# Kernel tuning notes

Hardware: AMD Instinct MI355X
Metric: run time of the kernel (lower is better)

The kernel has to match this reference:

```python
import jax, jax.numpy as jnp
import numpy as np

B, T, C, E, K = 8, 2048, 1024, 8, 2
CAP = int(T / E * 1.25)  # expert capacity per batch row = 320


def setup_inputs() -> dict:
    key = jax.random.key(0)
    ks = jax.random.split(key, 6)
    s = lambda k, shape, fan: jax.random.normal(k, shape, jnp.float32) / np.sqrt(fan)
    return dict(
        x=jax.random.normal(ks[0], (B, T, C), jnp.float32),
        rw1=s(ks[1], (C, 4 * C), C), rb1=jnp.zeros((4 * C,), jnp.float32),
        rw2=s(ks[2], (4 * C, 4 * C), 4 * C), rb2=jnp.zeros((4 * C,), jnp.float32),
        rw3=s(ks[3], (4 * C, E), 4 * C), rb3=jnp.zeros((E,), jnp.float32),
        ew1=s(ks[4], (E, C, 4 * C), C), eb1=jnp.zeros((E, 4 * C), jnp.float32),
        ew2=s(ks[5], (E, 4 * C, C), 4 * C), eb2=jnp.zeros((E, C), jnp.float32),
    )


def reference(x, rw1, rb1, rw2, rb2, rw3, rb3, ew1, eb1, ew2, eb2):
    # Router (dropout is identity in eval): MLP -> softmax over experts
    h = jax.nn.relu(x @ rw1 + rb1)
    h = jax.nn.relu(h @ rw2 + rb2)
    probs = jax.nn.softmax(h @ rw3 + rb3, axis=-1)        # [B,T,E]
    topk_p, topk_e = jax.lax.top_k(probs, K)              # [B,T,K]

    b_ids = jnp.broadcast_to(jnp.arange(B)[:, None], (B, T))
    out = jnp.zeros_like(x)
    # Loop over small fixed number of experts (mirrors per-rank expert compute)
    for e in range(E):
        sel = (topk_e == e)                               # [B,T,K]
        mask = sel.any(-1)                                # token routed to expert e
        gate = (topk_p * sel).sum(-1)                     # unnormalized top-k prob
        pos = jnp.cumsum(mask, axis=1) - 1                # slot within capacity buffer
        keep = mask & (pos < CAP)                         # capacity truncation (drop overflow)
        pos_s = jnp.where(keep, pos, CAP)                 # CAP is out-of-range -> dropped
        # Dispatch: scatter kept tokens into [B, CAP, C] capacity-padded buffer
        buf = jnp.zeros((B, CAP, C), x.dtype).at[b_ids, pos_s].set(x, mode='drop')
        # Expert FFN on padded buffer
        y = jax.nn.relu(buf @ ew1[e] + eb1[e]) @ ew2[e] + eb2[e]
        # Combine: gather back to token positions, weight by gate
        g = y[b_ids, jnp.where(keep, pos, 0)]
        out = out + gate[..., None] * jnp.where(keep[..., None], g, jnp.zeros((), x.dtype))
    return out
```

## Files before the change

### kernel.cpp

```cpp
#include <hip/hip_runtime.h>
#include <stdint.h>

typedef _Float16 f16;
typedef _Float16 half8 __attribute__((ext_vector_type(8)));
typedef float f32x4 __attribute__((ext_vector_type(4)));

#define NF_MAX 2048
#define THETA  0.02f

__device__ __forceinline__ void gload16(const void* g, void* l) {
  __builtin_amdgcn_global_load_lds(
      (const __attribute__((address_space(1))) void*)g,
      (__attribute__((address_space(3))) void*)l, 16, 0, 0);
}

#define BAR() do { __builtin_amdgcn_s_barrier(); __builtin_amdgcn_sched_barrier(0); } while (0)
#define WAIT_VM8() do { asm volatile("s_waitcnt vmcnt(8)" ::: "memory"); __builtin_amdgcn_sched_barrier(0); } while (0)
#define WAIT_VM0() do { asm volatile("s_waitcnt vmcnt(0)" ::: "memory"); __builtin_amdgcn_sched_barrier(0); } while (0)

template<int EPI, bool SPLIT3>
__launch_bounds__(512, 2)
__global__ void gemm256(const f16* __restrict__ A0, const f16* __restrict__ A1,
                        const f16* __restrict__ B0, const f16* __restrict__ B1,
                        int N, int Kd, int lda, int ldb,
                        const int* __restrict__ rowsrcA, const f16* __restrict__ zeroPage,
                        const float* __restrict__ bias, int bias_stride, int rows_per_exp,
                        f16* __restrict__ oH, int ldo, float* __restrict__ oAcc,
                        const float* __restrict__ w3, float* __restrict__ oLog,
                        const int* __restrict__ nfp)
{
  __shared__ f16 lds[4 * 8192 * 2 + 512];
  f16* sA = lds;
  f16* sB = lds + 4 * 8192;
  f16* sDummy = lds + 8 * 8192;

  const int tid  = threadIdx.x;
  const int lane = tid & 63, w = tid >> 6;
  const int wm = w >> 2, wn = w & 3;

  const int gx  = gridDim.x;
  const int nwg = gx * gridDim.y;
  const int bid = blockIdx.y * gx + blockIdx.x;
  const int swz = (bid & 7) * (nwg >> 3) + (bid >> 3);
  const int by  = swz / gx, bx = swz - by * gx;
  const int m0  = by * 256, n0 = bx * 256;
  const int k0  = blockIdx.z * Kd;

  if (nfp) {
    int nf = *nfp; nf = nf < NF_MAX ? nf : NF_MAX;
    const int lim = (nf + 255) & ~255;
    if (m0 >= lim) return;
  }

  int e = 0;
  if (rows_per_exp > 0) e = m0 / rows_per_exp;
  const f16* Bh = B0 + (size_t)e * N * ldb;

  const int nk  = Kd >> 6;
  const int NIT = SPLIT3 ? 3 * nk : nk;

  const int sr  = lane & 15;
  const int sk8 = lane >> 4;

  size_t aoff[2], boff[2];
  bool az[2] = { false, false };
  #pragma unroll
  for (int jj = 0; jj < 2; ++jj) {
    const int arow = m0 + (jj * 8 + w) * 16 + sr;
    if (rowsrcA) {
      const int rs = rowsrcA[arow];
      az[jj] = (rs < 0);
      aoff[jj] = az[jj] ? 0 : (size_t)rs * lda;
    } else {
      aoff[jj] = (size_t)arow * lda;
    }
    boff[jj] = (size_t)(n0 + (jj * 8 + w) * 16 + sr) * ldb;
  }

  auto stageA = [&](const f16* base, int kk, int kc, f16* slotBase, bool valid) {
    #pragma unroll
    for (int jj = 0; jj < 2; ++jj) {
      const int mt = jj * 8 + w;
      f16* dst = valid ? (slotBase + mt * 512) : sDummy;
      const f16* src = az[jj] ? zeroPage
                              : base + aoff[jj] + (k0 + kk + kc * 32 + sk8 * 8);
      gload16(src, dst);
    }
  };
  auto stageB = [&](const f16* base, int kk, int kc, f16* slotBase, bool valid) {
    #pragma unroll
    for (int jj = 0; jj < 2; ++jj) {
      const int mt = jj * 8 + w;
      f16* dst = valid ? (slotBase + mt * 512) : sDummy;
      const f16* src = base + boff[jj] + (k0 + kk + kc * 32 + sk8 * 8);
      gload16(src, dst);
    }
  };

  struct It { const f16* Ab; const f16* Bb; int kk, kin, pass; };
  const f16* Ab0 = SPLIT3 ? A1 : A0;
  auto advance = [&](It& s) {
    if (s.kin + 1 < nk) { s.kin++; }
    else if (SPLIT3 && s.pass < 2) {
      s.kin = 0; s.pass++;
      s.Ab = (s.pass == 0) ? A1 : A0;
      s.Bb = (s.pass == 1) ? B1 : Bh;
    }
    s.kk = s.kin << 6;
  };
  It it1 = { Ab0, Bh, 64, 1, 0 };
  It it2 = { Ab0, Bh, 128, 2, 0 };

  stageA(Ab0, 0, 0, &sA[0], true);
  stageB(Bh,  0, 0, &sB[0], true);
  stageA(Ab0, 0, 1, &sA[8192], true);
  stageB(Bh,  0, 1, &sB[8192], true);
  stageA(it1.Ab, it1.kk, 0, &sA[2 * 8192], true);
  stageB(it1.Bb, it1.kk, 0, &sB[2 * 8192], true);
  WAIT_VM8();
  BAR();

  f32x4 acc[8][4] = {};
  const int aBase = wm * 8;
  const int bBase = wn * 4;

  auto mfma16 = [&](half8* af, half8* bf, int moff) {
    __builtin_amdgcn_s_setprio(1);
    #pragma unroll
    for (int mi = 0; mi < 4; ++mi)
      #pragma unroll
      for (int ni = 0; ni < 4; ++ni)
        acc[moff + mi][ni] = __builtin_amdgcn_mfma_f32_16x16x32_f16(
            af[mi], bf[ni], acc[moff + mi][ni], 0, 0, 0);
    __builtin_amdgcn_s_setprio(0);
  };
  auto rdA = [&](half8* dst, int slot, int mtb) {
    #pragma unroll
    for (int mi = 0; mi < 4; ++mi)
      dst[mi] = *(const half8*)&sA[slot * 8192 + (mtb + mi) * 512 + lane * 8];
  };
  auto rdB = [&](half8* dst, int slot) {
    #pragma unroll
    for (int ni = 0; ni < 4; ++ni)
      dst[ni] = *(const half8*)&sB[slot * 8192 + (bBase + ni) * 512 + lane * 8];
  };

  for (int t = 0; t < NIT; ++t) {
    const int sa0 = (2 * t) & 3, sa1 = sa0 ^ 1;
    const bool v1 = (t + 1 < NIT), v2 = (t + 2 < NIT);

    if (SPLIT3 && t == 2 * nk) {
      #pragma unroll
      for (int mi = 0; mi < 8; ++mi)
        #pragma unroll
        for (int ni = 0; ni < 4; ++ni)
          acc[mi][ni] = acc[mi][ni] * 2.44140625e-4f;
    }

    half8 aF[4], bF[4], aG[4];

    rdA(aF, sa0, aBase);
    rdB(bF, sa0);
    stageA(it1.Ab, it1.kk, 1, &sA[(sa0 ^ 3) * 8192], v1);
    BAR();
    mfma16(aF, bF, 0);
    BAR();

    rdA(aG, sa0, aBase + 4);
    stageB(it1.Bb, it1.kk, 1, &sB[(sa0 ^ 3) * 8192], v1);
    WAIT_VM8();
    BAR();
    mfma16(aG, bF, 4);
    BAR();

    rdA(aF, sa1, aBase);
    rdB(bF, sa1);
    stageA(it2.Ab, it2.kk, 0, &sA[sa0 * 8192], v2);
    BAR();
    mfma16(aF, bF, 0);
    BAR();

    rdA(aG, sa1, aBase + 4);
    stageB(it2.Bb, it2.kk, 0, &sB[sa0 * 8192], v2);
    WAIT_VM8();
    BAR();
    mfma16(aG, bF, 4);
    BAR();

    it1 = it2;
    advance(it2);
  }
  WAIT_VM0();

  float bv[4] = { 0.f, 0.f, 0.f, 0.f };
  if (bias) {
    #pragma unroll
    for (int ni = 0; ni < 4; ++ni) {
      const int col = n0 + wn * 64 + ni * 16 + (lane & 15);
      bv[ni] = bias[(size_t)e * bias_stride + col];
    }
  }

  if (EPI == 2) {
    f32x4 wlo[4], whi[4];
    #pragma unroll
    for (int ni = 0; ni < 4; ++ni) {
      const int col = n0 + wn * 64 + ni * 16 + (lane & 15);
      wlo[ni] = *(const f32x4*)(w3 + (size_t)col * 8);
      whi[ni] = *(const f32x4*)(w3 + (size_t)col * 8 + 4);
    }
    const int p = (n0 >> 8) * 4 + wn;
    #pragma unroll
    for (int mi = 0; mi < 8; ++mi) {
      #pragma unroll
      for (int r = 0; r < 4; ++r) {
        const int row = m0 + wm * 128 + mi * 16 + (lane >> 4) * 4 + r;
        f32x4 plo = {}, phi = {};
        #pragma unroll
        for (int ni = 0; ni < 4; ++ni) {
          const float v = fmaxf(acc[mi][ni][r] + bv[ni], 0.f);
          plo += v * wlo[ni];
          phi += v * whi[ni];
        }
        #pragma unroll
        for (int msk = 1; msk < 16; msk <<= 1) {
          #pragma unroll
          for (int q = 0; q < 4; ++q) {
            plo[q] += __shfl_xor(plo[q], msk);
            phi[q] += __shfl_xor(phi[q], msk);
          }
        }
        if ((lane & 15) == 0) {
          float* dst = oLog + ((size_t)p * 4096 + row) * 8;
          *(f32x4*)dst = plo;
          *(f32x4*)(dst + 4) = phi;
        }
      }
    }
  } else {
    #pragma unroll
    for (int mi = 0; mi < 8; ++mi) {
      #pragma unroll
      for (int r = 0; r < 4; ++r) {
        const int row = m0 + wm * 128 + mi * 16 + (lane >> 4) * 4 + r;
        #pragma unroll
        for (int ni = 0; ni < 4; ++ni) {
          const int col = n0 + wn * 64 + ni * 16 + (lane & 15);
          if (EPI == 3) {
            atomicAdd(&oAcc[(size_t)row * ldo + col], acc[mi][ni][r]);
          } else {
            float v = acc[mi][ni][r] + bv[ni];
            if (EPI == 0) v = fmaxf(v, 0.f);
            oH[(size_t)row * ldo + col] = (f16)v;
          }
        }
      }
    }
  }
}

__global__ void split_x(const float* __restrict__ x, f16* __restrict__ hi,
                        f16* __restrict__ lo, int n)
{
  const int i = blockIdx.x * 256 + threadIdx.x;
  if (i * 8 >= n) return;
  const f32x4 a = ((const f32x4*)x)[2 * i];
  const f32x4 b = ((const f32x4*)x)[2 * i + 1];
  half8 h, l;
  #pragma unroll
  for (int j = 0; j < 4; ++j) {
    float v = a[j]; f16 hh = (f16)v;
    h[j] = hh; l[j] = (f16)((v - (float)hh) * 4096.0f);
    v = b[j]; hh = (f16)v;
    h[4 + j] = hh; l[4 + j] = (f16)((v - (float)hh) * 4096.0f);
  }
  ((half8*)hi)[i] = h;
  ((half8*)lo)[i] = l;
}

template<bool SPLIT>
__global__ void transpose_conv(const float* __restrict__ in, f16* __restrict__ oh,
                               f16* __restrict__ ol, int R, int Cc)
{
  __shared__ float tile[64][65];
  const size_t boff = (size_t)blockIdx.z * R * Cc;
  in += boff; oh += boff;
  if (SPLIT) ol += boff;
  const int c0 = blockIdx.x * 64, r0 = blockIdx.y * 64;
  #pragma unroll
  for (int i = 0; i < 16; ++i) {
    const int idx = i * 256 + threadIdx.x;
    const int r = idx >> 6, c = idx & 63;
    tile[r][c] = in[(size_t)(r0 + r) * Cc + (c0 + c)];
  }
  __syncthreads();
  #pragma unroll
  for (int i = 0; i < 16; ++i) {
    const int idx = i * 256 + threadIdx.x;
    const int ro = idx >> 6, co = idx & 63;
    const float v = tile[co][ro];
    const f16 h = (f16)v;
    const size_t o = (size_t)(c0 + ro) * R + (r0 + co);
    oh[o] = h;
    if (SPLIT) ol[o] = (f16)((v - (float)h) * 4096.0f);
  }
}

__global__ void topk_flag(const float* __restrict__ part, const float* __restrict__ b3,
                          int tok0, int* __restrict__ eidx, float* __restrict__ gval,
                          int* __restrict__ flags, int* __restrict__ nfc)
{
  const int tl = blockIdx.x * 256 + threadIdx.x;
  const int t  = tok0 + tl;
  float l[8];
  #pragma unroll
  for (int e = 0; e < 8; ++e) l[e] = b3[e];
  for (int p = 0; p < 64; ++p) {
    const float* src = part + ((size_t)p * 4096 + tl) * 8;
    const f32x4 a = *(const f32x4*)src;
    const f32x4 b = *(const f32x4*)(src + 4);
    #pragma unroll
    for (int q = 0; q < 4; ++q) { l[q] += a[q]; l[4 + q] += b[q]; }
  }
  float mx = l[0];
  #pragma unroll
  for (int e = 1; e < 8; ++e) mx = fmaxf(mx, l[e]);
  float ex[8], s = 0.f;
  #pragma unroll
  for (int e = 0; e < 8; ++e) { ex[e] = expf(l[e] - mx); s += ex[e]; }
  float p1 = -1.f, p2 = -1.f; int e1 = 0, e2 = 0;
  #pragma unroll
  for (int e = 0; e < 8; ++e) {
    const float pe = ex[e] / s;
    if (pe > p1)      { p2 = p1; e2 = e1; p1 = pe; e1 = e; }
    else if (pe > p2) { p2 = pe; e2 = e; }
  }
  eidx[t * 2] = e1; eidx[t * 2 + 1] = e2;
  gval[t * 2] = p1; gval[t * 2 + 1] = p2;
  float l1 = -1e30f, l2 = -1e30f, l3 = -1e30f;
  #pragma unroll
  for (int e = 0; e < 8; ++e) {
    const float le = l[e];
    if (le > l1)      { l3 = l2; l2 = l1; l1 = le; }
    else if (le > l2) { l3 = l2; l2 = le; }
    else if (le > l3) { l3 = le; }
  }
  if (l2 - l3 < THETA) {
    const int s0 = atomicAdd(nfc, 1);
    if (s0 < NF_MAX) flags[s0] = t;
  }
}

__global__ void post1(const float* __restrict__ h1r, const float* __restrict__ b1,
                      f16* __restrict__ hh, f16* __restrict__ hl,
                      const int* __restrict__ nfc)
{
  int nf = *nfc; nf = nf < NF_MAX ? nf : NF_MAX;
  const int lim = (nf + 255) & ~255;
  const int row = blockIdx.x;
  if (row >= lim) return;
  const int j = blockIdx.y * 2048 + threadIdx.x * 8;
  const float* src = h1r + (size_t)row * 4096 + j;
  const f32x4 a = *(const f32x4*)src;
  const f32x4 b = *(const f32x4*)(src + 4);
  half8 h, l;
  #pragma unroll
  for (int k = 0; k < 4; ++k) {
    float v = fmaxf(a[k] + b1[j + k], 0.f);
    f16 x = (f16)v; h[k] = x; l[k] = (f16)((v - (float)x) * 4096.0f);
    v = fmaxf(b[k] + b1[j + 4 + k], 0.f);
    x = (f16)v; h[4 + k] = x; l[4 + k] = (f16)((v - (float)x) * 4096.0f);
  }
  *(half8*)(hh + (size_t)row * 4096 + j) = h;
  *(half8*)(hl + (size_t)row * 4096 + j) = l;
}

__global__ void logits_exact(const float* __restrict__ h2r, const float* __restrict__ b2,
                             const float* __restrict__ w3, const float* __restrict__ b3,
                             const int* __restrict__ flags, const int* __restrict__ nfc,
                             int* __restrict__ eidx, float* __restrict__ gval)
{
  const int srow = blockIdx.x;
  int nf = *nfc; nf = nf < NF_MAX ? nf : NF_MAX;
  if (srow >= nf) return;
  const float* hrow = h2r + (size_t)srow * 4096;
  double p[8];
  #pragma unroll
  for (int e = 0; e < 8; ++e) p[e] = 0.0;
  for (int i = 0; i < 16; ++i) {
    const int k = i * 256 + threadIdx.x;
    const double h = (double)fmaxf(hrow[k] + b2[k], 0.f);
    const float* wp = w3 + (size_t)k * 8;
    #pragma unroll
    for (int e = 0; e < 8; ++e) p[e] += h * (double)wp[e];
  }
  #pragma unroll
  for (int e = 0; e < 8; ++e)
    for (int off = 32; off > 0; off >>= 1)
      p[e] += __shfl_down(p[e], off);
  __shared__ double sp[4][8];
  const int lane = threadIdx.x & 63, wv = threadIdx.x >> 6;
  if (lane == 0) {
    #pragma unroll
    for (int e = 0; e < 8; ++e) sp[wv][e] = p[e];
  }
  __syncthreads();
  if (threadIdx.x == 0) {
    float l[8];
    #pragma unroll
    for (int e = 0; e < 8; ++e)
      l[e] = (float)(sp[0][e] + sp[1][e] + sp[2][e] + sp[3][e] + (double)b3[e]);
    float mx = l[0];
    for (int e = 1; e < 8; ++e) mx = fmaxf(mx, l[e]);
    float ex[8], s = 0.f;
    for (int e = 0; e < 8; ++e) { ex[e] = expf(l[e] - mx); s += ex[e]; }
    float p1 = -1.f, p2 = -1.f; int e1 = 0, e2 = 0;
    for (int e = 0; e < 8; ++e) {
      const float pe = ex[e] / s;
      if (pe > p1)      { p2 = p1; e2 = e1; p1 = pe; e1 = e; }
      else if (pe > p2) { p2 = pe; e2 = e; }
    }
    const int tok = flags[srow];
    eidx[tok * 2] = e1; eidx[tok * 2 + 1] = e2;
    gval[tok * 2] = p1; gval[tok * 2 + 1] = p2;
  }
}

__global__ void route_scan(const int* __restrict__ eidx, const float* __restrict__ gval,
                           int* __restrict__ idxl, float* __restrict__ gatel,
                           int* __restrict__ cnt, int* __restrict__ rowsrc,
                           int* __restrict__ tokslot)
{
  const int pair = blockIdx.x;
  const int e = pair >> 3, b = pair & 7;
  const int lane = threadIdx.x;
  int running = 0;
  for (int t0 = 0; t0 < 2048; t0 += 64) {
    const int t = t0 + lane;
    const int i2 = (b * 2048 + t) * 2;
    const int m0 = (eidx[i2] == e), m1 = (eidx[i2 + 1] == e);
    const int m = m0 | m1;
    const float g = m0 ? gval[i2] : (m1 ? gval[i2 + 1] : 0.f);
    const unsigned long long bal = __ballot(m);
    const int pos = running + __popcll(bal & ((1ull << lane) - 1ull));
    if (m && pos < 320) {
      idxl[pair * 320 + pos] = t;
      gatel[pair * 320 + pos] = g;
      const int slot = pair * 320 + pos;
      rowsrc[slot] = b * 2048 + t;
      tokslot[(b * 2048 + t) * 2 + (m0 ? 0 : 1)] = slot;
    }
    running += __popcll(bal);
  }
  if (lane == 0) cnt[pair] = running < 320 ? running : 320;
}

__global__ void combine(const f16* __restrict__ yb, const int* __restrict__ tokslot,
                        const float* __restrict__ gval, float* __restrict__ out)
{
  const int t = blockIdx.x;
  const int s0 = tokslot[t * 2], s1 = tokslot[t * 2 + 1];
  const float g0 = gval[t * 2], g1 = gval[t * 2 + 1];
  float a[8] = {};
  if (s0 >= 0) {
    const half8 y = ((const half8*)(yb + (size_t)s0 * 1024))[threadIdx.x];
    #pragma unroll
    for (int k = 0; k < 8; ++k) a[k] += g0 * (float)y[k];
  }
  if (s1 >= 0) {
    const half8 y = ((const half8*)(yb + (size_t)s1 * 1024))[threadIdx.x];
    #pragma unroll
    for (int k = 0; k < 8; ++k) a[k] += g1 * (float)y[k];
  }
  float* dst = out + (size_t)t * 1024 + threadIdx.x * 8;
  f32x4 lo = { a[0], a[1], a[2], a[3] }, hi = { a[4], a[5], a[6], a[7] };
  *(f32x4*)dst = lo;
  *(f32x4*)(dst + 4) = hi;
}

extern "C" void kernel_launch(void* const* d_in, const int* in_sizes, int n_in,
                              void* d_out, int out_size, void* d_ws, size_t ws_size,
                              hipStream_t stream)
{
  (void)in_sizes; (void)n_in; (void)out_size;
  const float* x   = (const float*)d_in[0];
  const float* rw1 = (const float*)d_in[1];
  const float* rb1 = (const float*)d_in[2];
  const float* rw2 = (const float*)d_in[3];
  const float* rb2 = (const float*)d_in[4];
  const float* rw3 = (const float*)d_in[5];
  const float* rb3 = (const float*)d_in[6];
  const float* ew1 = (const float*)d_in[7];
  const float* eb1 = (const float*)d_in[8];
  const float* ew2 = (const float*)d_in[9];
  const float* eb2 = (const float*)d_in[10];

  constexpr size_t MB = 1024ull * 1024ull;
  constexpr size_t KB = 1024ull;
  char* ws = (char*)d_ws;
  if (ws_size < 401 * MB) return;

  f16*   ew1t  = (f16*)(ws);
  f16*   ew2t  = (f16*)(ws + 64 * MB);
  f16*   xhi   = (f16*)(ws + 128 * MB);
  char*  S     = ws + 160 * MB;
  int*   eidx   = (int*)(S);
  float* gval   = (float*)(S + 128 * KB);
  int*   idxl   = (int*)(S + 256 * KB);
  float* gatel  = (float*)(S + 352 * KB);
  int*   cnt    = (int*)(S + 448 * KB);
  int*   nfc    = (int*)(S + 452 * KB);
  int*   flags  = (int*)(S + 456 * KB);
  int*   tokslot= (int*)(S + 464 * KB);
  int*   rowsrc = (int*)(S + 592 * KB);
  f16*   zeros  = (f16*)(S + 688 * KB);
  f16*   xlo    = (f16*)(ws + 162 * MB);
  f16*   rw1thi = (f16*)(ws + 194 * MB);
  f16*   rw1tlo = (f16*)(ws + 202 * MB);
  f16*   rw2thi = (f16*)(ws + 210 * MB);
  f16*   rw2tlo = (f16*)(ws + 242 * MB);
  f16*   h1f    = (f16*)(ws + 274 * MB);
  float* h1r    = (float*)(ws + 274 * MB);
  float* h2r    = (float*)(ws + 306 * MB);
  f16*   h1rh   = (f16*)(ws + 338 * MB);
  f16*   h1rl   = (f16*)(ws + 354 * MB);
  float* part   = (float*)(ws + 390 * MB);
  f16*   h_e    = (f16*)(ws + 162 * MB);
  f16*   yb     = (f16*)(ws + 322 * MB);

  hipMemsetAsync(nfc, 0, 4, stream);
  hipMemsetAsync(flags, 0, 8 * KB, stream);
  hipMemsetAsync(tokslot, 0xFF, 128 * KB, stream);
  hipMemsetAsync(rowsrc, 0xFF, 80 * KB, stream);
  hipMemsetAsync(zeros, 0, 16 * KB, stream);

  split_x<<<8192, 256, 0, stream>>>(x, xhi, xlo, 16384 * 1024);
  transpose_conv<true ><<<dim3(64, 16, 1), 256, 0, stream>>>(rw1, rw1thi, rw1tlo, 1024, 4096);
  transpose_conv<true ><<<dim3(64, 64, 1), 256, 0, stream>>>(rw2, rw2thi, rw2tlo, 4096, 4096);
  transpose_conv<false><<<dim3(64, 16, 8), 256, 0, stream>>>(ew1, ew1t, nullptr, 1024, 4096);
  transpose_conv<false><<<dim3(16, 64, 8), 256, 0, stream>>>(ew2, ew2t, nullptr, 4096, 1024);

  for (int c = 0; c < 4; ++c) {
    const f16* xh = xhi + (size_t)c * 4096 * 1024;
    gemm256<0, false><<<dim3(16, 16), 512, 0, stream>>>(
        xh, nullptr, rw1thi, nullptr, 4096, 1024, 1024, 1024,
        nullptr, nullptr, rb1, 0, 0,
        h1f, 4096, nullptr, nullptr, nullptr, nullptr);
    gemm256<2, false><<<dim3(16, 16), 512, 0, stream>>>(
        h1f, nullptr, rw2thi, nullptr, 4096, 4096, 4096, 4096,
        nullptr, nullptr, rb2, 0, 0,
        nullptr, 0, nullptr, rw3, part, nullptr);
    topk_flag<<<16, 256, 0, stream>>>(part, rb3, c * 4096, eidx, gval, flags, nfc);
  }

  hipMemsetAsync(h1r, 0, 32 * MB, stream);
  hipMemsetAsync(h2r, 0, 32 * MB, stream);
  gemm256<3, true><<<dim3(16, 8, 2), 512, 0, stream>>>(
      xhi, xlo, rw1thi, rw1tlo, 4096, 512, 1024, 1024,
      flags, zeros, nullptr, 0, 0,
      nullptr, 4096, h1r, nullptr, nullptr, nfc);
  post1<<<dim3(2048, 2), 256, 0, stream>>>(h1r, rb1, h1rh, h1rl, nfc);
  gemm256<3, true><<<dim3(16, 8, 4), 512, 0, stream>>>(
      h1rh, h1rl, rw2thi, rw2tlo, 4096, 1024, 4096, 4096,
      nullptr, nullptr, nullptr, 0, 0,
      nullptr, 4096, h2r, nullptr, nullptr, nfc);
  logits_exact<<<NF_MAX, 256, 0, stream>>>(h2r, rb2, rw3, rb3, flags, nfc,
                                           eidx, gval);

  route_scan<<<64, 64, 0, stream>>>(eidx, gval, idxl, gatel, cnt, rowsrc, tokslot);

  gemm256<0, false><<<dim3(16, 80), 512, 0, stream>>>(
      xhi, nullptr, ew1t, nullptr, 4096, 1024, 1024, 1024,
      rowsrc, zeros, eb1, 4096, 2560,
      h_e, 4096, nullptr, nullptr, nullptr, nullptr);
  gemm256<1, false><<<dim3(4, 80), 512, 0, stream>>>(
      h_e, nullptr, ew2t, nullptr, 1024, 4096, 4096, 4096,
      nullptr, nullptr, eb2, 1024, 2560,
      yb, 1024, nullptr, nullptr, nullptr, nullptr);

  combine<<<16384, 128, 0, stream>>>(yb, tokslot, gval, (float*)d_out);
}
```

Baseline: 1.830 ms.

## Merge router chunks into full-size GEMMs and split-K expert down projection

Replaces the four per-chunk router GEMM and top-k launches with single full-batch launches over all 16384 tokens, relaying out workspace buffers to fit. The expert second GEMM becomes a 4-way split-K with fp32 atomic accumulation into a zeroed buffer, and bias is added in combine. It also hoists an LDS fragment read earlier in the GEMM main loop, removes unused routing outputs, and moves expert weight transposes later. The aim is better GPU fill and fewer launches, at the cost of atomics, extra memsets, and larger fp32 intermediates.

```diff
diff --git a/kernel.cpp b/kernel.cpp
--- a/kernel.cpp
+++ b/kernel.cpp
@@ -161,12 +161,12 @@
 
     rdA(aF, sa0, aBase);
     rdB(bF, sa0);
+    rdA(aG, sa0, aBase + 4);
     stageA(it1.Ab, it1.kk, 1, &sA[(sa0 ^ 3) * 8192], v1);
     BAR();
     mfma16(aF, bF, 0);
     BAR();
 
-    rdA(aG, sa0, aBase + 4);
     stageB(it1.Bb, it1.kk, 1, &sB[(sa0 ^ 3) * 8192], v1);
     WAIT_VM8();
     BAR();
@@ -175,12 +175,12 @@
 
     rdA(aF, sa1, aBase);
     rdB(bF, sa1);
+    rdA(aG, sa1, aBase + 4);
     stageA(it2.Ab, it2.kk, 0, &sA[sa0 * 8192], v2);
     BAR();
     mfma16(aF, bF, 0);
     BAR();
 
-    rdA(aG, sa1, aBase + 4);
     stageB(it2.Bb, it2.kk, 0, &sB[sa0 * 8192], v2);
     WAIT_VM8();
     BAR();
@@ -231,7 +231,7 @@
           }
         }
         if ((lane & 15) == 0) {
-          float* dst = oLog + ((size_t)p * 4096 + row) * 8;
+          float* dst = oLog + ((size_t)p * ldo + row) * 8;
           *(f32x4*)dst = plo;
           *(f32x4*)(dst + 4) = phi;
         }
@@ -307,16 +307,15 @@
 }
 
 __global__ void topk_flag(const float* __restrict__ part, const float* __restrict__ b3,
-                          int tok0, int* __restrict__ eidx, float* __restrict__ gval,
+                          int* __restrict__ eidx, float* __restrict__ gval,
                           int* __restrict__ flags, int* __restrict__ nfc)
 {
-  const int tl = blockIdx.x * 256 + threadIdx.x;
-  const int t  = tok0 + tl;
+  const int t = blockIdx.x * 256 + threadIdx.x;
   float l[8];
   #pragma unroll
   for (int e = 0; e < 8; ++e) l[e] = b3[e];
   for (int p = 0; p < 64; ++p) {
-    const float* src = part + ((size_t)p * 4096 + tl) * 8;
+    const float* src = part + ((size_t)p * 16384 + t) * 8;
     const f32x4 a = *(const f32x4*)src;
     const f32x4 b = *(const f32x4*)(src + 4);
     #pragma unroll
@@ -427,7 +426,6 @@
 }
 
 __global__ void route_scan(const int* __restrict__ eidx, const float* __restrict__ gval,
-                           int* __restrict__ idxl, float* __restrict__ gatel,
                            int* __restrict__ cnt, int* __restrict__ rowsrc,
                            int* __restrict__ tokslot)
 {
@@ -440,42 +438,44 @@
     const int i2 = (b * 2048 + t) * 2;
     const int m0 = (eidx[i2] == e), m1 = (eidx[i2 + 1] == e);
     const int m = m0 | m1;
-    const float g = m0 ? gval[i2] : (m1 ? gval[i2 + 1] : 0.f);
     const unsigned long long bal = __ballot(m);
     const int pos = running + __popcll(bal & ((1ull << lane) - 1ull));
     if (m && pos < 320) {
-      idxl[pair * 320 + pos] = t;
-      gatel[pair * 320 + pos] = g;
       const int slot = pair * 320 + pos;
       rowsrc[slot] = b * 2048 + t;
       tokslot[(b * 2048 + t) * 2 + (m0 ? 0 : 1)] = slot;
     }
     running += __popcll(bal);
   }
-  if (lane == 0) cnt[pair] = running < 320 ? running : 320;
-}
-
-__global__ void combine(const f16* __restrict__ yb, const int* __restrict__ tokslot,
-                        const float* __restrict__ gval, float* __restrict__ out)
+  const int c = running < 320 ? running : 320;
+  for (int s = c + lane; s < 320; s += 64) rowsrc[pair * 320 + s] = -1;
+  if (lane == 0) cnt[pair] = c;
+}
+
+__global__ void combine(const float* __restrict__ ybF, const int* __restrict__ tokslot,
+                        const float* __restrict__ gval, const float* __restrict__ eb2,
+                        float* __restrict__ out)
 {
   const int t = blockIdx.x;
+  const int c = threadIdx.x * 8;
   const int s0 = tokslot[t * 2], s1 = tokslot[t * 2 + 1];
   const float g0 = gval[t * 2], g1 = gval[t * 2 + 1];
-  float a[8] = {};
+  f32x4 a0 = {}, a1 = {};
   if (s0 >= 0) {
-    const half8 y = ((const half8*)(yb + (size_t)s0 * 1024))[threadIdx.x];
-    #pragma unroll
-    for (int k = 0; k < 8; ++k) a[k] += g0 * (float)y[k];
+    const float* y = ybF + (size_t)s0 * 1024 + c;
+    const float* bb = eb2 + (size_t)(s0 / 2560) * 1024 + c;
+    a0 += g0 * (*(const f32x4*)y + *(const f32x4*)bb);
+    a1 += g0 * (*(const f32x4*)(y + 4) + *(const f32x4*)(bb + 4));
   }
   if (s1 >= 0) {
-    const half8 y = ((const half8*)(yb + (size_t)s1 * 1024))[threadIdx.x];
-    #pragma unroll
-    for (int k = 0; k < 8; ++k) a[k] += g1 * (float)y[k];
-  }
-  float* dst = out + (size_t)t * 1024 + threadIdx.x * 8;
-  f32x4 lo = { a[0], a[1], a[2], a[3] }, hi = { a[4], a[5], a[6], a[7] };
-  *(f32x4*)dst = lo;
-  *(f32x4*)(dst + 4) = hi;
+    const float* y = ybF + (size_t)s1 * 1024 + c;
+    const float* bb = eb2 + (size_t)(s1 / 2560) * 1024 + c;
+    a0 += g1 * (*(const f32x4*)y + *(const f32x4*)bb);
+    a1 += g1 * (*(const f32x4*)(y + 4) + *(const f32x4*)(bb + 4));
+  }
+  float* dst = out + (size_t)t * 1024 + c;
+  *(f32x4*)dst = a0;
+  *(f32x4*)(dst + 4) = a1;
 }
 
 extern "C" void kernel_launch(void* const* d_in, const int* in_sizes, int n_in,
@@ -500,61 +500,51 @@
   char* ws = (char*)d_ws;
   if (ws_size < 401 * MB) return;
 
-  f16*   ew1t  = (f16*)(ws);
-  f16*   ew2t  = (f16*)(ws + 64 * MB);
-  f16*   xhi   = (f16*)(ws + 128 * MB);
-  char*  S     = ws + 160 * MB;
+  f16*   h1f  = (f16*)(ws);
+  f16*   ew1t = (f16*)(ws);
+  f16*   ew2t = (f16*)(ws + 64 * MB);
+  f16*   xhi  = (f16*)(ws + 128 * MB);
+  char*  S    = ws + 160 * MB;
   int*   eidx   = (int*)(S);
   float* gval   = (float*)(S + 128 * KB);
-  int*   idxl   = (int*)(S + 256 * KB);
-  float* gatel  = (float*)(S + 352 * KB);
-  int*   cnt    = (int*)(S + 448 * KB);
-  int*   nfc    = (int*)(S + 452 * KB);
-  int*   flags  = (int*)(S + 456 * KB);
-  int*   tokslot= (int*)(S + 464 * KB);
-  int*   rowsrc = (int*)(S + 592 * KB);
-  f16*   zeros  = (f16*)(S + 688 * KB);
-  f16*   xlo    = (f16*)(ws + 162 * MB);
-  f16*   rw1thi = (f16*)(ws + 194 * MB);
-  f16*   rw1tlo = (f16*)(ws + 202 * MB);
-  f16*   rw2thi = (f16*)(ws + 210 * MB);
-  f16*   rw2tlo = (f16*)(ws + 242 * MB);
-  f16*   h1f    = (f16*)(ws + 274 * MB);
-  float* h1r    = (float*)(ws + 274 * MB);
-  float* h2r    = (float*)(ws + 306 * MB);
-  f16*   h1rh   = (f16*)(ws + 338 * MB);
-  f16*   h1rl   = (f16*)(ws + 354 * MB);
-  float* part   = (float*)(ws + 390 * MB);
-  f16*   h_e    = (f16*)(ws + 162 * MB);
-  f16*   yb     = (f16*)(ws + 322 * MB);
+  int*   cnt    = (int*)(S + 256 * KB);
+  int*   nfc    = (int*)(S + 260 * KB);
+  int*   flags  = (int*)(S + 264 * KB);
+  int*   tokslot= (int*)(S + 272 * KB);
+  int*   rowsrc = (int*)(S + 400 * KB);
+  f16*   zeros  = (f16*)(S + 480 * KB);
+  f16*   xlo    = (f16*)(ws + 161 * MB);
+  f16*   rw1thi = (f16*)(ws + 193 * MB);
+  f16*   rw1tlo = (f16*)(ws + 201 * MB);
+  f16*   rw2thi = (f16*)(ws + 209 * MB);
+  f16*   rw2tlo = (f16*)(ws + 241 * MB);
+  float* part   = (float*)(ws + 273 * MB);
+  float* h1r    = (float*)(ws + 305 * MB);
+  float* h2r    = (float*)(ws + 337 * MB);
+  f16*   h1rh   = (f16*)(ws + 369 * MB);
+  f16*   h1rl   = (f16*)(ws + 385 * MB);
+  f16*   h_e    = (f16*)(ws + 161 * MB);
+  float* ybF    = (float*)(ws + 321 * MB);
 
   hipMemsetAsync(nfc, 0, 4, stream);
-  hipMemsetAsync(flags, 0, 8 * KB, stream);
   hipMemsetAsync(tokslot, 0xFF, 128 * KB, stream);
-  hipMemsetAsync(rowsrc, 0xFF, 80 * KB, stream);
   hipMemsetAsync(zeros, 0, 16 * KB, stream);
+  hipMemsetAsync(h1r, 0, 64 * MB, stream);
 
   split_x<<<8192, 256, 0, stream>>>(x, xhi, xlo, 16384 * 1024);
   transpose_conv<true ><<<dim3(64, 16, 1), 256, 0, stream>>>(rw1, rw1thi, rw1tlo, 1024, 4096);
   transpose_conv<true ><<<dim3(64, 64, 1), 256, 0, stream>>>(rw2, rw2thi, rw2tlo, 4096, 4096);
-  transpose_conv<false><<<dim3(64, 16, 8), 256, 0, stream>>>(ew1, ew1t, nullptr, 1024, 4096);
-  transpose_conv<false><<<dim3(16, 64, 8), 256, 0, stream>>>(ew2, ew2t, nullptr, 4096, 1024);
-
-  for (int c = 0; c < 4; ++c) {
-    const f16* xh = xhi + (size_t)c * 4096 * 1024;
-    gemm256<0, false><<<dim3(16, 16), 512, 0, stream>>>(
-        xh, nullptr, rw1thi, nullptr, 4096, 1024, 1024, 1024,
-        nullptr, nullptr, rb1, 0, 0,
-        h1f, 4096, nullptr, nullptr, nullptr, nullptr);
-    gemm256<2, false><<<dim3(16, 16), 512, 0, stream>>>(
-        h1f, nullptr, rw2thi, nullptr, 4096, 4096, 4096, 4096,
-        nullptr, nullptr, rb2, 0, 0,
-        nullptr, 0, nullptr, rw3, part, nullptr);
-    topk_flag<<<16, 256, 0, stream>>>(part, rb3, c * 4096, eidx, gval, flags, nfc);
-  }
-
-  hipMemsetAsync(h1r, 0, 32 * MB, stream);
-  hipMemsetAsync(h2r, 0, 32 * MB, stream);
+
+  gemm256<0, false><<<dim3(16, 64), 512, 0, stream>>>(
+      xhi, nullptr, rw1thi, nullptr, 4096, 1024, 1024, 1024,
+      nullptr, nullptr, rb1, 0, 0,
+      h1f, 4096, nullptr, nullptr, nullptr, nullptr);
+  gemm256<2, false><<<dim3(16, 64), 512, 0, stream>>>(
+      h1f, nullptr, rw2thi, nullptr, 4096, 4096, 4096, 4096,
+      nullptr, nullptr, rb2, 0, 0,
+      nullptr, 16384, nullptr, rw3, part, nullptr);
+  topk_flag<<<64, 256, 0, stream>>>(part, rb3, eidx, gval, flags, nfc);
+
   gemm256<3, true><<<dim3(16, 8, 2), 512, 0, stream>>>(
       xhi, xlo, rw1thi, rw1tlo, 4096, 512, 1024, 1024,
       flags, zeros, nullptr, 0, 0,
@@ -567,16 +557,20 @@
   logits_exact<<<NF_MAX, 256, 0, stream>>>(h2r, rb2, rw3, rb3, flags, nfc,
                                            eidx, gval);
 
-  route_scan<<<64, 64, 0, stream>>>(eidx, gval, idxl, gatel, cnt, rowsrc, tokslot);
+  route_scan<<<64, 64, 0, stream>>>(eidx, gval, cnt, rowsrc, tokslot);
+
+  transpose_conv<false><<<dim3(64, 16, 8), 256, 0, stream>>>(ew1, ew1t, nullptr, 1024, 4096);
+  transpose_conv<false><<<dim3(16, 64, 8), 256, 0, stream>>>(ew2, ew2t, nullptr, 4096, 1024);
+  hipMemsetAsync(ybF, 0, 80 * MB, stream);
 
   gemm256<0, false><<<dim3(16, 80), 512, 0, stream>>>(
       xhi, nullptr, ew1t, nullptr, 4096, 1024, 1024, 1024,
       rowsrc, zeros, eb1, 4096, 2560,
       h_e, 4096, nullptr, nullptr, nullptr, nullptr);
-  gemm256<1, false><<<dim3(4, 80), 512, 0, stream>>>(
-      h_e, nullptr, ew2t, nullptr, 1024, 4096, 4096, 4096,
-      nullptr, nullptr, eb2, 1024, 2560,
-      yb, 1024, nullptr, nullptr, nullptr, nullptr);
-
-  combine<<<16384, 128, 0, stream>>>(yb, tokslot, gval, (float*)d_out);
-}
+  gemm256<3, false><<<dim3(4, 80, 4), 512, 0, stream>>>(
+      h_e, nullptr, ew2t, nullptr, 1024, 1024, 4096, 4096,
+      nullptr, nullptr, nullptr, 0, 2560,
+      nullptr, 1024, ybF, nullptr, nullptr, nullptr);
+
+  combine<<<16384, 128, 0, stream>>>(ybF, tokslot, gval, eb2, (float*)d_out);
+}
```

After: 1.894 ms. 3.5% more time.
